# Kernel tuning notes

Measured on AMD Instinct MI355X. Metric: run time of the kernel, lower is better.

Reference implementation:

```python
import jax, jax.numpy as jnp
import numpy as np
from jax.scipy.special import logsumexp

SCALE = 10.0
EPS = 1e-05
MARGIN_INTRA = 40.0
MARGIN_INTER = 6.0
K_INTRA = 4   # sorted1[4:]
K_INTER = 6   # sorted2[6:]


def setup_inputs() -> dict:
    key = jax.random.key(0)
    k1, k2 = jax.random.split(key)
    n, d, n_cams = 4096, 256, 8
    feature = jax.random.normal(k1, (n, d), dtype=jnp.float32)
    camid = jax.random.randint(k2, (n,), 0, n_cams, dtype=jnp.int64)
    return {"feature": feature, "camid": camid}


def reference(feature, camid):
    n = feature.shape[0]
    # pairwise Euclidean distances: ||fi||^2 + ||fj||^2 - 2 fi.fj + eps, clamped, sqrt
    sq = jnp.sum(feature * feature, axis=1)                      # [n]
    dist = sq[:, None] + sq[None, :] + EPS - 2.0 * (feature @ feature.T)
    dist = jnp.sqrt(jnp.clip(dist, 1e-12))                       # [n, n]

    same_cam = camid[:, None] == camid[None, :]                  # [n, n] bool
    inf = jnp.array(jnp.inf, dtype=dist.dtype)

    # masked sorts: +inf padding sorts to the end and contributes exp(-inf)=0
    sorted_intra = jnp.sort(jnp.where(same_cam, dist, inf), axis=1)   # [n, n]
    sorted_inter = jnp.sort(jnp.where(same_cam, inf, dist), axis=1)   # [n, n]

    # x = log(sum(exp(-scale * sorted[:1]))) == -scale * sorted[0]
    x_intra = -SCALE * sorted_intra[:, 0]
    y_intra = logsumexp(-SCALE * sorted_intra[:, K_INTRA:], axis=1)
    x_inter = -SCALE * sorted_inter[:, 0]
    y_inter = logsumexp(-SCALE * sorted_inter[:, K_INTER:], axis=1)

    loss_intra = jnp.sum(jnp.maximum(-x_intra + y_intra + MARGIN_INTRA, 0.0))
    loss_inter = jnp.sum(jnp.maximum(-x_inter + y_inter + MARGIN_INTER, 0.0))
    return (loss_intra + 0.5 * loss_inter) / n
```

## Files before the change

kernel.cpp:

```cpp
#include <hip/hip_runtime.h>
#include <hip/hip_bf16.h>
#include <math.h>

#define N 4096
#define D 256
#define SCALEF 10.0f
#define EPSF 1e-5f
#define MARGIN_INTRA 40.0f
#define MARGIN_INTER 6.0f
#define LI 3
#define LX 6
#define NCHUNK 16
#define NSTRIP 32
#define PPARTS (NCHUNK * 2)

#define LOG2EF 1.44269504f
#define LN2F 0.69314718f

typedef unsigned short ushort_t;
typedef __attribute__((ext_vector_type(8))) short short8;
typedef __attribute__((ext_vector_type(4))) float floatx4;

__device__ __forceinline__ ushort_t f2bf(float x) {
    __hip_bfloat16 h = __float2bfloat16(x);
    return *reinterpret_cast<ushort_t*>(&h);
}
__device__ __forceinline__ float bf2f(ushort_t u) {
    __hip_bfloat16 h = *reinterpret_cast<__hip_bfloat16*>(&u);
    return __bfloat162float(h);
}

__device__ __forceinline__ float fast_exp2(float x) {
#if __has_builtin(__builtin_amdgcn_exp2f)
    return __builtin_amdgcn_exp2f(x);
#else
    return exp2f(x);
#endif
}

template <int L>
__device__ __forceinline__ void insert_desc(float (&t)[L], float v) {
    float top = fmaxf(t[0], v);
#pragma unroll
    for (int q = L - 1; q >= 1; --q)
        t[q] = __builtin_amdgcn_fmed3f(t[q - 1], t[q], v);
    t[0] = top;
}

__global__ __launch_bounds__(64) void prep_kernel(const float* __restrict__ F,
                                                  ushort_t* __restrict__ Fhi,
                                                  ushort_t* __restrict__ Flo,
                                                  float* __restrict__ sq,
                                                  float* __restrict__ Rrow) {
    int row = blockIdx.x;
    int lane = threadIdx.x;
    float4 v = ((const float4*)(F + (size_t)row * D))[lane];
    ushort4 h, l;
    h.x = f2bf(v.x); l.x = f2bf(v.x - bf2f(h.x));
    h.y = f2bf(v.y); l.y = f2bf(v.y - bf2f(h.y));
    h.z = f2bf(v.z); l.z = f2bf(v.z - bf2f(h.z));
    h.w = f2bf(v.w); l.w = f2bf(v.w - bf2f(h.w));
    ((ushort4*)(Fhi + (size_t)row * D))[lane] = h;
    ((ushort4*)(Flo + (size_t)row * D))[lane] = l;
    float s = v.x * v.x + v.y * v.y + v.z * v.z + v.w * v.w;
#pragma unroll
    for (int off = 32; off > 0; off >>= 1) s += __shfl_down(s, off, 64);
    if (lane == 0) {
        sq[row] = s;
        Rrow[row] = -SCALEF * sqrtf(2.0f * s);
    }
}

#define LDST 40

template <bool HD>
__device__ __forceinline__ void epi_tile(
    const floatx4 (&acc)[4][4], int j0, int wr, int quad,
    const float (&si)[4], const float (&nR2)[4], const int (&ci4)[4], const int (&ig)[4],
    const float* __restrict__ sq, const int* __restrict__ camid,
    float (&tI)[4][LI], float (&tX)[4][LX], float (&sIa)[4], float (&sXa)[4]) {
    const float C1 = -SCALEF * LOG2EF;
#pragma unroll
    for (int mi = 0; mi < 4; ++mi) {
        int jg0 = j0 + wr * 64 + mi * 16 + quad * 4;
        float4 sj4 = *(const float4*)(sq + jg0);
        int4 cj4 = *(const int4*)(camid + jg0);
        const float* sjp = (const float*)&sj4;
        const int* cjp = (const int*)&cj4;
#pragma unroll
        for (int ni = 0; ni < 4; ++ni) {
            int dd = jg0 - ig[ni];
            float sie = si[ni] + EPSF;
#pragma unroll
            for (int r = 0; r < 4; ++r) {
                float d2 = sie + sjp[r] - 2.0f * acc[mi][ni][r];
                float d = sqrtf(fmaxf(d2, 1e-12f));
                float k = fmaf(d, C1, nR2[ni]);
                float e = fast_exp2(k);
                bool ii = (cjp[r] == ci4[ni]);
                bool okI = HD ? (ii && ((dd + r) != 0)) : ii;
                sIa[ni] += okI ? e : 0.0f;
                sXa[ni] += ii ? 0.0f : e;
                insert_desc<LI>(tI[ni], okI ? k : -INFINITY);
                insert_desc<LX>(tX[ni], ii ? -INFINITY : k);
            }
        }
    }
}

__global__ __launch_bounds__(256, 2) void fused_kernel(
    const ushort_t* __restrict__ Fhi, const ushort_t* __restrict__ Flo,
    const float* __restrict__ sq, const float* __restrict__ Rrow,
    const int* __restrict__ camid,
    float4* __restrict__ partA, float4* __restrict__ partB, float4* __restrict__ partC) {
    __shared__ ushort_t lds[4][128 * LDST];
    int tid = threadIdx.x;
    int wave = tid >> 6, lane = tid & 63;
    int wr = wave >> 1, wc = wave & 1;
    int lane15 = lane & 15, quad = lane >> 4;
    int cid = blockIdx.x, sid = blockIdx.y;
    int i0 = sid * 128, j00 = cid * 256;

    float si[4], nR2[4];
    int ci4[4], ig[4];
#pragma unroll
    for (int ni = 0; ni < 4; ++ni) {
        int i = i0 + wc * 64 + ni * 16 + lane15;
        ig[ni] = i;
        si[ni] = sq[i];
        nR2[ni] = -Rrow[i] * LOG2EF;
        ci4[ni] = camid[i];
    }

    float tI[4][LI], tX[4][LX], sIa[4], sXa[4];
#pragma unroll
    for (int ni = 0; ni < 4; ++ni) {
#pragma unroll
        for (int q = 0; q < LI; ++q) tI[ni][q] = -INFINITY;
#pragma unroll
        for (int q = 0; q < LX; ++q) tX[ni][q] = -INFINITY;
        sIa[ni] = 0.0f; sXa[ni] = 0.0f;
    }

    int srow = tid >> 1, shalf = tid & 1;
    const ushort_t* gBh = Fhi + (size_t)(i0 + srow) * D + shalf * 16;
    const ushort_t* gBl = Flo + (size_t)(i0 + srow) * D + shalf * 16;
    ushort_t* sdst = &lds[0][0] + srow * LDST + shalf * 16;

#pragma unroll 1
    for (int jt = 0; jt < 2; ++jt) {
        int j0 = j00 + jt * 128;
        const ushort_t* gAh = Fhi + (size_t)(j0 + srow) * D + shalf * 16;
        const ushort_t* gAl = Flo + (size_t)(j0 + srow) * D + shalf * 16;
        floatx4 acc[4][4] = {};

#pragma unroll 1
        for (int kt = 0; kt < 8; ++kt) {
            int koff = kt * 32;
            short8 ra[2], rb[2], rc[2], rd[2];
#pragma unroll
            for (int q = 0; q < 2; ++q) {
                ra[q] = *(const short8*)(gAh + koff + q * 8);
                rb[q] = *(const short8*)(gAl + koff + q * 8);
                rc[q] = *(const short8*)(gBh + koff + q * 8);
                rd[q] = *(const short8*)(gBl + koff + q * 8);
            }
            __syncthreads();
#pragma unroll
            for (int q = 0; q < 2; ++q) {
                *(short8*)(sdst + 0 * 128 * LDST + q * 8) = ra[q];
                *(short8*)(sdst + 1 * 128 * LDST + q * 8) = rb[q];
                *(short8*)(sdst + 2 * 128 * LDST + q * 8) = rc[q];
                *(short8*)(sdst + 3 * 128 * LDST + q * 8) = rd[q];
            }
            __syncthreads();

            short8 ahi[4], alo[4], bhi[4], blo[4];
            int eoff = quad * 8;
#pragma unroll
            for (int mi = 0; mi < 4; ++mi) {
                int r = wr * 64 + mi * 16 + lane15;
                ahi[mi] = *(const short8*)(&lds[0][0] + r * LDST + eoff);
                alo[mi] = *(const short8*)(&lds[1][0] + r * LDST + eoff);
            }
#pragma unroll
            for (int ni = 0; ni < 4; ++ni) {
                int r = wc * 64 + ni * 16 + lane15;
                bhi[ni] = *(const short8*)(&lds[2][0] + r * LDST + eoff);
                blo[ni] = *(const short8*)(&lds[3][0] + r * LDST + eoff);
            }
#pragma unroll
            for (int mi = 0; mi < 4; ++mi)
#pragma unroll
                for (int ni = 0; ni < 4; ++ni) {
                    acc[mi][ni] = __builtin_amdgcn_mfma_f32_16x16x32_bf16(ahi[mi], bhi[ni], acc[mi][ni], 0, 0, 0);
                    acc[mi][ni] = __builtin_amdgcn_mfma_f32_16x16x32_bf16(ahi[mi], blo[ni], acc[mi][ni], 0, 0, 0);
                    acc[mi][ni] = __builtin_amdgcn_mfma_f32_16x16x32_bf16(alo[mi], bhi[ni], acc[mi][ni], 0, 0, 0);
                }
        }

        if (cid == (sid >> 1) && jt == (sid & 1))
            epi_tile<true>(acc, j0, wr, quad, si, nR2, ci4, ig, sq, camid, tI, tX, sIa, sXa);
        else
            epi_tile<false>(acc, j0, wr, quad, si, nR2, ci4, ig, sq, camid, tI, tX, sIa, sXa);
    }

#pragma unroll
    for (int off = 16; off <= 32; off <<= 1) {
#pragma unroll
        for (int ni = 0; ni < 4; ++ni) {
            sIa[ni] += __shfl_xor(sIa[ni], off, 64);
            sXa[ni] += __shfl_xor(sXa[ni], off, 64);
            float oI[LI], oX[LX];
#pragma unroll
            for (int q = 0; q < LI; ++q) oI[q] = __shfl_xor(tI[ni][q], off, 64);
#pragma unroll
            for (int q = 0; q < LX; ++q) oX[q] = __shfl_xor(tX[ni][q], off, 64);
#pragma unroll
            for (int q = 0; q < LI; ++q) insert_desc<LI>(tI[ni], oI[q]);
#pragma unroll
            for (int q = 0; q < LX; ++q) insert_desc<LX>(tX[ni], oX[q]);
        }
    }

    if (quad == 0) {
        int p = cid * 2 + wr;
#pragma unroll
        for (int ni = 0; ni < 4; ++ni) {
            size_t idx = (size_t)p * N + ig[ni];
            partA[idx] = make_float4(tI[ni][0], tI[ni][1], tI[ni][2], sIa[ni]);
            partB[idx] = make_float4(tX[ni][0], tX[ni][1], tX[ni][2], tX[ni][3]);
            partC[idx] = make_float4(tX[ni][4], tX[ni][5], sXa[ni], 0.0f);
        }
    }
}

__global__ __launch_bounds__(256) void merge_kernel(const float4* __restrict__ partA,
                                                    const float4* __restrict__ partB,
                                                    const float4* __restrict__ partC,
                                                    const float* __restrict__ Rrow,
                                                    float* __restrict__ rowloss) {
    int row = blockIdx.x * 256 + threadIdx.x;
    float mI[LI] = {-INFINITY, -INFINITY, -INFINITY};
    float mX[LX] = {-INFINITY, -INFINITY, -INFINITY, -INFINITY, -INFINITY, -INFINITY};
    float SI = 0.0f, SX = 0.0f;
#pragma unroll 4
    for (int p = 0; p < PPARTS; ++p) {
        size_t idx = (size_t)p * N + row;
        float4 a = partA[idx];
        float4 b = partB[idx];
        float4 c = partC[idx];
        insert_desc<LI>(mI, a.x); insert_desc<LI>(mI, a.y); insert_desc<LI>(mI, a.z);
        SI += a.w;
        insert_desc<LX>(mX, b.x); insert_desc<LX>(mX, b.y);
        insert_desc<LX>(mX, b.z); insert_desc<LX>(mX, b.w);
        insert_desc<LX>(mX, c.x); insert_desc<LX>(mX, c.y);
        SX += c.z;
    }
    float R = Rrow[row];
    float subI = fast_exp2(mI[0]) + fast_exp2(mI[1]) + fast_exp2(mI[2]);
    float restI = fmaxf(SI - subI, 1e-37f);
    float yI = R + logf(restI);
    float hI = fmaxf(yI + SCALEF * sqrtf(EPSF) + MARGIN_INTRA, 0.0f);
    float subX = fast_exp2(mX[0]) + fast_exp2(mX[1]) + fast_exp2(mX[2]) +
                 fast_exp2(mX[3]) + fast_exp2(mX[4]) + fast_exp2(mX[5]);
    float restX = fmaxf(SX - subX, 1e-37f);
    float hX = fmaxf(logf(restX) - mX[0] * LN2F + MARGIN_INTER, 0.0f);
    rowloss[row] = hI + 0.5f * hX;
}

__global__ __launch_bounds__(256) void final_reduce(const float* __restrict__ rowloss,
                                                    float* __restrict__ out) {
    __shared__ float sbuf[256];
    int tid = threadIdx.x;
    float acc = 0.0f;
#pragma unroll
    for (int s = 0; s < 16; ++s) acc += rowloss[tid + s * 256];
    sbuf[tid] = acc;
    __syncthreads();
    for (int stride = 128; stride > 0; stride >>= 1) {
        if (tid < stride) sbuf[tid] += sbuf[tid + stride];
        __syncthreads();
    }
    if (tid == 0) out[0] = sbuf[0] * (1.0f / (float)N);
}

extern "C" void kernel_launch(void* const* d_in, const int* in_sizes, int n_in,
                              void* d_out, int out_size, void* d_ws, size_t ws_size,
                              hipStream_t stream) {
    const float* F = (const float*)d_in[0];
    const int* camid = (const int*)d_in[1];
    float* out = (float*)d_out;
    char* ws = (char*)d_ws;

    ushort_t* Fhi = (ushort_t*)ws;
    ushort_t* Flo = Fhi + (size_t)N * D;
    float* sq = (float*)(ws + 2 * (size_t)N * D * 2);
    float* Rrow = sq + N;
    float* rowloss = Rrow + N;
    float4* partA = (float4*)(ws + 2 * (size_t)N * D * 2 + 3 * N * 4);
    float4* partB = partA + (size_t)PPARTS * N;
    float4* partC = partB + (size_t)PPARTS * N;

    prep_kernel<<<N, 64, 0, stream>>>(F, Fhi, Flo, sq, Rrow);
    fused_kernel<<<dim3(NCHUNK, NSTRIP), 256, 0, stream>>>(Fhi, Flo, sq, Rrow, camid,
                                                           partA, partB, partC);
    merge_kernel<<<N / 256, 256, 0, stream>>>(partA, partB, partC, Rrow, rowloss);
    final_reduce<<<1, 256, 0, stream>>>(rowloss, out);
}
```

Baseline: 120.2 us.

## Halve row-strip tile to 64 rows for higher occupancy and fold final reduce into merge

The fused distance/top-k kernel now covers 64 query rows per block instead of 128, which doubles the grid and cuts per-thread accumulator and top-k register state so the launch bound can request four blocks per SIMD instead of two. The B-tile LDS staging is reshaped to match the smaller strip. Separately, the single-block final reduce kernel is removed: each merge block reduces its rows in LDS and atomically adds into the output, which prep_kernel zeroes. This trades more A-tile reloads across the doubled grid, and a float atomic sum whose order is nondeterministic, for better latency hiding and one fewer launch.

```diff
diff --git a/kernel.cpp b/kernel.cpp
--- a/kernel.cpp
+++ b/kernel.cpp
@@ -11,7 +11,7 @@
 #define LI 3
 #define LX 6
 #define NCHUNK 16
-#define NSTRIP 32
+#define NSTRIP 64
 #define PPARTS (NCHUNK * 2)
 
 #define LOG2EF 1.44269504f
@@ -51,9 +51,11 @@
                                                   ushort_t* __restrict__ Fhi,
                                                   ushort_t* __restrict__ Flo,
                                                   float* __restrict__ sq,
-                                                  float* __restrict__ Rrow) {
+                                                  float* __restrict__ Rrow,
+                                                  float* __restrict__ out) {
     int row = blockIdx.x;
     int lane = threadIdx.x;
+    if (row == 0 && lane == 0) out[0] = 0.0f;
     float4 v = ((const float4*)(F + (size_t)row * D))[lane];
     ushort4 h, l;
     h.x = f2bf(v.x); l.x = f2bf(v.x - bf2f(h.x));
@@ -75,10 +77,10 @@
 
 template <bool HD>
 __device__ __forceinline__ void epi_tile(
-    const floatx4 (&acc)[4][4], int j0, int wr, int quad,
-    const float (&si)[4], const float (&nR2)[4], const int (&ci4)[4], const int (&ig)[4],
+    const floatx4 (&acc)[4][2], int j0, int wr, int quad,
+    const float (&si)[2], const float (&nR2)[2], const int (&ci4)[2], const int (&ig)[2],
     const float* __restrict__ sq, const int* __restrict__ camid,
-    float (&tI)[4][LI], float (&tX)[4][LX], float (&sIa)[4], float (&sXa)[4]) {
+    float (&tI)[2][LI], float (&tX)[2][LX], float (&sIa)[2], float (&sXa)[2]) {
     const float C1 = -SCALEF * LOG2EF;
 #pragma unroll
     for (int mi = 0; mi < 4; ++mi) {
@@ -88,7 +90,7 @@
         const float* sjp = (const float*)&sj4;
         const int* cjp = (const int*)&cj4;
 #pragma unroll
-        for (int ni = 0; ni < 4; ++ni) {
+        for (int ni = 0; ni < 2; ++ni) {
             int dd = jg0 - ig[ni];
             float sie = si[ni] + EPSF;
 #pragma unroll
@@ -108,33 +110,38 @@
     }
 }
 
-__global__ __launch_bounds__(256, 2) void fused_kernel(
+__global__ __launch_bounds__(256, 4) void fused_kernel(
     const ushort_t* __restrict__ Fhi, const ushort_t* __restrict__ Flo,
     const float* __restrict__ sq, const float* __restrict__ Rrow,
     const int* __restrict__ camid,
     float4* __restrict__ partA, float4* __restrict__ partB, float4* __restrict__ partC) {
-    __shared__ ushort_t lds[4][128 * LDST];
+    __shared__ ushort_t lds[(128 + 128 + 64 + 64) * LDST];
+    ushort_t* ldsAh = lds;
+    ushort_t* ldsAl = lds + 128 * LDST;
+    ushort_t* ldsBh = lds + 256 * LDST;
+    ushort_t* ldsBl = lds + 320 * LDST;
+
     int tid = threadIdx.x;
     int wave = tid >> 6, lane = tid & 63;
     int wr = wave >> 1, wc = wave & 1;
     int lane15 = lane & 15, quad = lane >> 4;
     int cid = blockIdx.x, sid = blockIdx.y;
-    int i0 = sid * 128, j00 = cid * 256;
-
-    float si[4], nR2[4];
-    int ci4[4], ig[4];
-#pragma unroll
-    for (int ni = 0; ni < 4; ++ni) {
-        int i = i0 + wc * 64 + ni * 16 + lane15;
+    int i0 = sid * 64, j00 = cid * 256;
+
+    float si[2], nR2[2];
+    int ci4[2], ig[2];
+#pragma unroll
+    for (int ni = 0; ni < 2; ++ni) {
+        int i = i0 + wc * 32 + ni * 16 + lane15;
         ig[ni] = i;
         si[ni] = sq[i];
         nR2[ni] = -Rrow[i] * LOG2EF;
         ci4[ni] = camid[i];
     }
 
-    float tI[4][LI], tX[4][LX], sIa[4], sXa[4];
-#pragma unroll
-    for (int ni = 0; ni < 4; ++ni) {
+    float tI[2][LI], tX[2][LX], sIa[2], sXa[2];
+#pragma unroll
+    for (int ni = 0; ni < 2; ++ni) {
 #pragma unroll
         for (int q = 0; q < LI; ++q) tI[ni][q] = -INFINITY;
 #pragma unroll
@@ -142,64 +149,66 @@
         sIa[ni] = 0.0f; sXa[ni] = 0.0f;
     }
 
-    int srow = tid >> 1, shalf = tid & 1;
-    const ushort_t* gBh = Fhi + (size_t)(i0 + srow) * D + shalf * 16;
-    const ushort_t* gBl = Flo + (size_t)(i0 + srow) * D + shalf * 16;
-    ushort_t* sdst = &lds[0][0] + srow * LDST + shalf * 16;
+    int srowA = tid >> 1, shalf = tid & 1;
+    int srowB = tid >> 2, squart = tid & 3;
+    const ushort_t* gBh = Fhi + (size_t)(i0 + srowB) * D + squart * 8;
+    const ushort_t* gBl = Flo + (size_t)(i0 + srowB) * D + squart * 8;
+    ushort_t* sdstAh = ldsAh + srowA * LDST + shalf * 16;
+    ushort_t* sdstAl = ldsAl + srowA * LDST + shalf * 16;
+    ushort_t* sdstBh = ldsBh + srowB * LDST + squart * 8;
+    ushort_t* sdstBl = ldsBl + srowB * LDST + squart * 8;
 
 #pragma unroll 1
     for (int jt = 0; jt < 2; ++jt) {
         int j0 = j00 + jt * 128;
-        const ushort_t* gAh = Fhi + (size_t)(j0 + srow) * D + shalf * 16;
-        const ushort_t* gAl = Flo + (size_t)(j0 + srow) * D + shalf * 16;
-        floatx4 acc[4][4] = {};
+        const ushort_t* gAh = Fhi + (size_t)(j0 + srowA) * D + shalf * 16;
+        const ushort_t* gAl = Flo + (size_t)(j0 + srowA) * D + shalf * 16;
+        floatx4 acc[4][2] = {};
 
 #pragma unroll 1
         for (int kt = 0; kt < 8; ++kt) {
             int koff = kt * 32;
-            short8 ra[2], rb[2], rc[2], rd[2];
+            short8 ra[2], rb[2], rc, rd;
 #pragma unroll
             for (int q = 0; q < 2; ++q) {
                 ra[q] = *(const short8*)(gAh + koff + q * 8);
                 rb[q] = *(const short8*)(gAl + koff + q * 8);
-                rc[q] = *(const short8*)(gBh + koff + q * 8);
-                rd[q] = *(const short8*)(gBl + koff + q * 8);
-            }
+            }
+            rc = *(const short8*)(gBh + koff);
+            rd = *(const short8*)(gBl + koff);
             __syncthreads();
 #pragma unroll
             for (int q = 0; q < 2; ++q) {
-                *(short8*)(sdst + 0 * 128 * LDST + q * 8) = ra[q];
-                *(short8*)(sdst + 1 * 128 * LDST + q * 8) = rb[q];
-                *(short8*)(sdst + 2 * 128 * LDST + q * 8) = rc[q];
-                *(short8*)(sdst + 3 * 128 * LDST + q * 8) = rd[q];
-            }
+                *(short8*)(sdstAh + q * 8) = ra[q];
+                *(short8*)(sdstAl + q * 8) = rb[q];
+            }
+            *(short8*)(sdstBh) = rc;
+            *(short8*)(sdstBl) = rd;
             __syncthreads();
 
-            short8 ahi[4], alo[4], bhi[4], blo[4];
             int eoff = quad * 8;
+            short8 ahi[4], alo[4];
 #pragma unroll
             for (int mi = 0; mi < 4; ++mi) {
                 int r = wr * 64 + mi * 16 + lane15;
-                ahi[mi] = *(const short8*)(&lds[0][0] + r * LDST + eoff);
-                alo[mi] = *(const short8*)(&lds[1][0] + r * LDST + eoff);
-            }
-#pragma unroll
-            for (int ni = 0; ni < 4; ++ni) {
-                int r = wc * 64 + ni * 16 + lane15;
-                bhi[ni] = *(const short8*)(&lds[2][0] + r * LDST + eoff);
-                blo[ni] = *(const short8*)(&lds[3][0] + r * LDST + eoff);
-            }
-#pragma unroll
-            for (int mi = 0; mi < 4; ++mi)
-#pragma unroll
-                for (int ni = 0; ni < 4; ++ni) {
-                    acc[mi][ni] = __builtin_amdgcn_mfma_f32_16x16x32_bf16(ahi[mi], bhi[ni], acc[mi][ni], 0, 0, 0);
-                    acc[mi][ni] = __builtin_amdgcn_mfma_f32_16x16x32_bf16(ahi[mi], blo[ni], acc[mi][ni], 0, 0, 0);
-                    acc[mi][ni] = __builtin_amdgcn_mfma_f32_16x16x32_bf16(alo[mi], bhi[ni], acc[mi][ni], 0, 0, 0);
+                ahi[mi] = *(const short8*)(ldsAh + r * LDST + eoff);
+                alo[mi] = *(const short8*)(ldsAl + r * LDST + eoff);
+            }
+#pragma unroll
+            for (int ni = 0; ni < 2; ++ni) {
+                int r = wc * 32 + ni * 16 + lane15;
+                short8 bhi = *(const short8*)(ldsBh + r * LDST + eoff);
+                short8 blo = *(const short8*)(ldsBl + r * LDST + eoff);
+#pragma unroll
+                for (int mi = 0; mi < 4; ++mi) {
+                    acc[mi][ni] = __builtin_amdgcn_mfma_f32_16x16x32_bf16(ahi[mi], bhi, acc[mi][ni], 0, 0, 0);
+                    acc[mi][ni] = __builtin_amdgcn_mfma_f32_16x16x32_bf16(ahi[mi], blo, acc[mi][ni], 0, 0, 0);
+                    acc[mi][ni] = __builtin_amdgcn_mfma_f32_16x16x32_bf16(alo[mi], bhi, acc[mi][ni], 0, 0, 0);
                 }
+            }
         }
 
-        if (cid == (sid >> 1) && jt == (sid & 1))
+        if (cid == (sid >> 2) && jt == ((sid >> 1) & 1))
             epi_tile<true>(acc, j0, wr, quad, si, nR2, ci4, ig, sq, camid, tI, tX, sIa, sXa);
         else
             epi_tile<false>(acc, j0, wr, quad, si, nR2, ci4, ig, sq, camid, tI, tX, sIa, sXa);
@@ -208,7 +217,7 @@
 #pragma unroll
     for (int off = 16; off <= 32; off <<= 1) {
 #pragma unroll
-        for (int ni = 0; ni < 4; ++ni) {
+        for (int ni = 0; ni < 2; ++ni) {
             sIa[ni] += __shfl_xor(sIa[ni], off, 64);
             sXa[ni] += __shfl_xor(sXa[ni], off, 64);
             float oI[LI], oX[LX];
@@ -226,7 +235,7 @@
     if (quad == 0) {
         int p = cid * 2 + wr;
 #pragma unroll
-        for (int ni = 0; ni < 4; ++ni) {
+        for (int ni = 0; ni < 2; ++ni) {
             size_t idx = (size_t)p * N + ig[ni];
             partA[idx] = make_float4(tI[ni][0], tI[ni][1], tI[ni][2], sIa[ni]);
             partB[idx] = make_float4(tX[ni][0], tX[ni][1], tX[ni][2], tX[ni][3]);
@@ -239,8 +248,9 @@
                                                     const float4* __restrict__ partB,
                                                     const float4* __restrict__ partC,
                                                     const float* __restrict__ Rrow,
-                                                    float* __restrict__ rowloss) {
-    int row = blockIdx.x * 256 + threadIdx.x;
+                                                    float* __restrict__ out) {
+    int tid = threadIdx.x;
+    int row = blockIdx.x * 256 + tid;
     float mI[LI] = {-INFINITY, -INFINITY, -INFINITY};
     float mX[LX] = {-INFINITY, -INFINITY, -INFINITY, -INFINITY, -INFINITY, -INFINITY};
     float SI = 0.0f, SX = 0.0f;
@@ -266,23 +276,16 @@
                  fast_exp2(mX[3]) + fast_exp2(mX[4]) + fast_exp2(mX[5]);
     float restX = fmaxf(SX - subX, 1e-37f);
     float hX = fmaxf(logf(restX) - mX[0] * LN2F + MARGIN_INTER, 0.0f);
-    rowloss[row] = hI + 0.5f * hX;
-}
-
-__global__ __launch_bounds__(256) void final_reduce(const float* __restrict__ rowloss,
-                                                    float* __restrict__ out) {
+    float l = hI + 0.5f * hX;
+
     __shared__ float sbuf[256];
-    int tid = threadIdx.x;
-    float acc = 0.0f;
-#pragma unroll
-    for (int s = 0; s < 16; ++s) acc += rowloss[tid + s * 256];
-    sbuf[tid] = acc;
+    sbuf[tid] = l;
     __syncthreads();
     for (int stride = 128; stride > 0; stride >>= 1) {
         if (tid < stride) sbuf[tid] += sbuf[tid + stride];
         __syncthreads();
     }
-    if (tid == 0) out[0] = sbuf[0] * (1.0f / (float)N);
+    if (tid == 0) atomicAdd(out, sbuf[0] * (1.0f / (float)N));
 }
 
 extern "C" void kernel_launch(void* const* d_in, const int* in_sizes, int n_in,
@@ -298,13 +301,13 @@
     float* sq = (float*)(ws + 2 * (size_t)N * D * 2);
     float* Rrow = sq + N;
     float* rowloss = Rrow + N;
+    (void)rowloss;
     float4* partA = (float4*)(ws + 2 * (size_t)N * D * 2 + 3 * N * 4);
     float4* partB = partA + (size_t)PPARTS * N;
     float4* partC = partB + (size_t)PPARTS * N;
 
-    prep_kernel<<<N, 64, 0, stream>>>(F, Fhi, Flo, sq, Rrow);
+    prep_kernel<<<N, 64, 0, stream>>>(F, Fhi, Flo, sq, Rrow, out);
     fused_kernel<<<dim3(NCHUNK, NSTRIP), 256, 0, stream>>>(Fhi, Flo, sq, Rrow, camid,
                                                            partA, partB, partC);
-    merge_kernel<<<N / 256, 256, 0, stream>>>(partA, partB, partC, Rrow, rowloss);
-    final_reduce<<<1, 256, 0, stream>>>(rowloss, out);
-}
+    merge_kernel<<<N / 256, 256, 0, stream>>>(partA, partB, partC, Rrow, out);
+}
```

After: 127.6 us. +6.2%, slower.
